# Performance work log

Measured on AMD Instinct MI355X. Metric: run time of the kernel, lower is better.

The kernel has to match this reference:

```python
import jax, jax.numpy as jnp
import numpy as np

INPUT_SIZE = 256
HIDDEN = 512

def setup_inputs() -> dict:
    key = jax.random.key(0)
    ks = jax.random.split(key, 12)
    B, T, I, H = 64, 1024, INPUT_SIZE, HIDDEN
    s = 1.0 / np.sqrt(I + H)
    x = jax.random.normal(ks[0], (B, T, I), dtype=jnp.float32)
    Wf = jax.random.uniform(ks[1], (I + H, H), jnp.float32, -s, s)
    bf = jax.random.uniform(ks[2], (H,), jnp.float32, -s, s)
    Wi = jax.random.uniform(ks[3], (I + H, H), jnp.float32, -s, s)
    bi = jax.random.uniform(ks[4], (H,), jnp.float32, -s, s)
    Wc = jax.random.uniform(ks[5], (I + H, H), jnp.float32, -s, s)
    bc = jax.random.uniform(ks[6], (H,), jnp.float32, -s, s)
    Wo = jax.random.uniform(ks[7], (I + H, H), jnp.float32, -s, s)
    bo = jax.random.uniform(ks[8], (H,), jnp.float32, -s, s)
    sf = 1.0 / np.sqrt(H)
    W_fc = jax.random.uniform(ks[9], (H, 1), jnp.float32, -sf, sf)
    b_fc = jax.random.uniform(ks[10], (1,), jnp.float32, -sf, sf)
    return {"x": x, "Wf": Wf, "bf": bf, "Wi": Wi, "bi": bi,
            "Wc": Wc, "bc": bc, "Wo": Wo, "bo": bo,
            "W_fc": W_fc, "b_fc": b_fc}

def reference(x, Wf, bf, Wi, bi, Wc, bc, Wo, bo, W_fc, b_fc):
    B, T, I = x.shape
    H = Wf.shape[1]
    # Fuse the 4 gate GEMMs into one [I+H, 4H] matmul (same math, one launch).
    W = jnp.concatenate([Wf, Wi, Wc, Wo], axis=1)   # [I+H, 4H]
    b = jnp.concatenate([bf, bi, bc, bo], axis=0)   # [4H]
    h0 = jnp.zeros((B, H), x.dtype)
    c0 = jnp.zeros((B, H), x.dtype)

    def step(carry, xt):
        h, c = carry
        combined = jnp.concatenate([xt, h], axis=1)     # [B, I+H]
        gates = combined @ W + b                        # [B, 4H]
        f, i, c_tilde, o = jnp.split(gates, 4, axis=1)
        f = jax.nn.sigmoid(f)
        i = jax.nn.sigmoid(i)
        c_tilde = jnp.tanh(c_tilde)
        o = jax.nn.sigmoid(o)
        c = f * c + i * c_tilde
        h = o * jnp.tanh(c)
        return (h, c), None

    (h, c), _ = jax.lax.scan(step, (h0, c0), jnp.swapaxes(x, 0, 1))
    return h @ W_fc + b_fc  # [B, 1]
```

## Files before the change

kernel.cpp:

```cpp
#include <hip/hip_runtime.h>
#include <hip/hip_fp16.h>


#define T_STEPS 1024
#define BATCH   64
#define ISZ     256
#define HSZ     512
#define NWG     128
#define NTHR    256
#define HB4     ((BATCH * HSZ) / 4)

typedef _Float16 half8  __attribute__((ext_vector_type(8)));
typedef _Float16 half4  __attribute__((ext_vector_type(4)));
typedef float    floatx4 __attribute__((ext_vector_type(4)));
typedef unsigned long long u64;

#define LD_AGENT(p)     __hip_atomic_load((p), __ATOMIC_RELAXED, __HIP_MEMORY_SCOPE_AGENT)
#define ST_AGENT(p, v)  __hip_atomic_store((p), (v), __ATOMIC_RELAXED, __HIP_MEMORY_SCOPE_AGENT)

__device__ __forceinline__ float fast_sigmoid(float x) {
    return 1.0f / (1.0f + __expf(-x));
}
__device__ __forceinline__ float fast_tanh(float x) {
    return 1.0f - 2.0f / (__expf(2.0f * x) + 1.0f);
}

__global__ __launch_bounds__(NTHR, 1) void lstm_persist(
    const float* __restrict__ x,
    const float* __restrict__ Wf, const float* __restrict__ bfv,
    const float* __restrict__ Wi, const float* __restrict__ biv,
    const float* __restrict__ Wc, const float* __restrict__ bcv,
    const float* __restrict__ Wo, const float* __restrict__ bov,
    u64* __restrict__ hbuf4, unsigned* __restrict__ flags)
{
    const int g    = blockIdx.x;
    const int tid  = threadIdx.x;
    const int w    = tid >> 6;
    const int l    = tid & 63;
    const int lj   = l & 15;
    const int lk   = l >> 4;
    const int gate = lj >> 2;
    const int jc   = lj & 3;
    const int hc   = (g << 2) + jc;
    const int row0 = w << 4;
    const int arow = row0 + lj;

    const float* Wg = (gate == 0) ? Wf : (gate == 1) ? Wi : (gate == 2) ? Wc : Wo;
    const float* bg = (gate == 0) ? bfv : (gate == 1) ? biv : (gate == 2) ? bcv : bov;

    half8 Bfrag[24];
    #pragma unroll
    for (int kf = 0; kf < 24; ++kf) {
        half8 v;
        #pragma unroll
        for (int e = 0; e < 8; ++e) {
            int k = (kf << 5) + (lk << 3) + e;
            v[e] = (_Float16)Wg[(size_t)k * HSZ + hc];
        }
        Bfrag[kf] = v;
    }
    const float bias = bg[hc];
    float cst[4] = {0.f, 0.f, 0.f, 0.f};

    const u64* fl = (const u64*)flags;

    floatx4 accx = {0.f, 0.f, 0.f, 0.f};
    {
        const float* xr = x + (size_t)arow * T_STEPS * ISZ + (lk << 3);
        #pragma unroll
        for (int kf = 0; kf < 8; ++kf) {
            floatx4 x0 = *(const floatx4*)(xr + (kf << 5));
            floatx4 x1 = *(const floatx4*)(xr + (kf << 5) + 4);
            half8 a;
            a[0] = (_Float16)x0[0]; a[1] = (_Float16)x0[1];
            a[2] = (_Float16)x0[2]; a[3] = (_Float16)x0[3];
            a[4] = (_Float16)x1[0]; a[5] = (_Float16)x1[1];
            a[6] = (_Float16)x1[2]; a[7] = (_Float16)x1[3];
            accx = __builtin_amdgcn_mfma_f32_16x16x32_f16(a, Bfrag[kf], accx, 0, 0, 0);
        }
    }

    for (int t = 0; t < T_STEPS; ++t) {
        floatx4 acc0, acc1;
        #pragma unroll
        for (int e = 0; e < 4; ++e) { acc0[e] = accx[e] + bias; acc1[e] = 0.f; }

        if (t > 0) {
            if (w == 0) {
                const unsigned tgt = (unsigned)t;
                while (true) {
                    u64 v = LD_AGENT(fl + l);
                    if (__all(((unsigned)v >= tgt) && ((unsigned)(v >> 32) >= tgt))) break;
                    __builtin_amdgcn_s_sleep(1);
                }
            }
            __syncthreads();

            const u64* hr = hbuf4 + (size_t)(t & 1) * HB4 + arow;
            u64 hl[32];
            #pragma unroll
            for (int kf = 0; kf < 16; ++kf) {
                const int c0 = kf * 8 + lk * 2;
                hl[2 * kf]     = LD_AGENT(hr + (size_t)c0 * BATCH);
                hl[2 * kf + 1] = LD_AGENT(hr + (size_t)(c0 + 1) * BATCH);
            }
            #pragma unroll
            for (int kf = 0; kf < 16; kf += 2) {
                union { u64 u[2]; half8 h; } a0, a1;
                a0.u[0] = hl[2 * kf];     a0.u[1] = hl[2 * kf + 1];
                a1.u[0] = hl[2 * kf + 2]; a1.u[1] = hl[2 * kf + 3];
                acc0 = __builtin_amdgcn_mfma_f32_16x16x32_f16(a0.h, Bfrag[8 + kf], acc0, 0, 0, 0);
                acc1 = __builtin_amdgcn_mfma_f32_16x16x32_f16(a1.h, Bfrag[9 + kf], acc1, 0, 0, 0);
            }
        }

        floatx4 act;
        if (gate == 2) {
            #pragma unroll
            for (int e = 0; e < 4; ++e) act[e] = fast_tanh(acc0[e] + acc1[e]);
        } else {
            #pragma unroll
            for (int e = 0; e < 4; ++e) act[e] = fast_sigmoid(acc0[e] + acc1[e]);
        }

        const int base = l & ~12;
        float hv[4];
        #pragma unroll
        for (int e = 0; e < 4; ++e) {
            float vf = __shfl(act[e], base);
            float vi = __shfl(act[e], base + 4);
            float vc = __shfl(act[e], base + 8);
            float vo = __shfl(act[e], base + 12);
            float c  = vf * cst[e] + vi * vc;
            cst[e] = c;
            hv[e] = vo * fast_tanh(c);
        }

        half4 outv;
        #pragma unroll
        for (int col = 0; col < 4; ++col) {
            const int src = ((l & 15) >> 2) * 16 + col;
            float sel = 0.f;
            #pragma unroll
            for (int e = 0; e < 4; ++e) {
                float tmp = __shfl(hv[e], src);
                if ((l & 3) == e) sel = tmp;
            }
            outv[col] = (_Float16)sel;
        }
        u64* hw = hbuf4 + (size_t)((t + 1) & 1) * HB4 + (size_t)g * BATCH + row0;
        if (l < 16) {
            union { half4 h; u64 u; } pk; pk.h = outv;
            ST_AGENT(hw + l, pk.u);
        }
        asm volatile("s_waitcnt vmcnt(0)" ::: "memory");
        __syncthreads();
        if (tid == 0) ST_AGENT(&flags[g], (unsigned)(t + 1));

        if (t + 1 < T_STEPS) {
            floatx4 az = {0.f, 0.f, 0.f, 0.f};
            const float* xr = x + ((size_t)arow * T_STEPS + (t + 1)) * ISZ + (lk << 3);
            #pragma unroll
            for (int kf = 0; kf < 8; ++kf) {
                floatx4 x0 = *(const floatx4*)(xr + (kf << 5));
                floatx4 x1 = *(const floatx4*)(xr + (kf << 5) + 4);
                half8 a;
                a[0] = (_Float16)x0[0]; a[1] = (_Float16)x0[1];
                a[2] = (_Float16)x0[2]; a[3] = (_Float16)x0[3];
                a[4] = (_Float16)x1[0]; a[5] = (_Float16)x1[1];
                a[6] = (_Float16)x1[2]; a[7] = (_Float16)x1[3];
                az = __builtin_amdgcn_mfma_f32_16x16x32_f16(a, Bfrag[kf], az, 0, 0, 0);
            }
            accx = az;
        }
    }
}

__global__ void out_proj(const u64* __restrict__ hb4, const float* __restrict__ Wfc,
                         const float* __restrict__ bfc, float* __restrict__ out)
{
    const int b = blockIdx.x;
    const int l = threadIdx.x;
    float s = 0.f;
    #pragma unroll
    for (int j = 0; j < 2; ++j) {
        const int c4 = l + (j << 6);
        union { u64 u; half4 h; } v;
        v.u = hb4[(size_t)c4 * BATCH + b];
        #pragma unroll
        for (int q = 0; q < 4; ++q)
            s += (float)v.h[q] * Wfc[c4 * 4 + q];
    }
    #pragma unroll
    for (int off = 32; off; off >>= 1) s += __shfl_down(s, off);
    if (l == 0) out[b] = s + bfc[0];
}

extern "C" void kernel_launch(void* const* d_in, const int* in_sizes, int n_in,
                              void* d_out, int out_size, void* d_ws, size_t ws_size,
                              hipStream_t stream)
{
    const float* x   = (const float*)d_in[0];
    const float* Wf  = (const float*)d_in[1];
    const float* bf  = (const float*)d_in[2];
    const float* Wi  = (const float*)d_in[3];
    const float* bi  = (const float*)d_in[4];
    const float* Wc  = (const float*)d_in[5];
    const float* bc  = (const float*)d_in[6];
    const float* Wo  = (const float*)d_in[7];
    const float* bo  = (const float*)d_in[8];
    const float* Wfc = (const float*)d_in[9];
    const float* bfc = (const float*)d_in[10];

    u64* hbuf4 = (u64*)d_ws;
    unsigned* flags = (unsigned*)((char*)d_ws + 2 * HB4 * sizeof(u64));

    hipMemsetAsync(flags, 0, NWG * sizeof(unsigned), stream);

    void* args[] = { (void*)&x, (void*)&Wf, (void*)&bf, (void*)&Wi, (void*)&bi,
                     (void*)&Wc, (void*)&bc, (void*)&Wo, (void*)&bo,
                     (void*)&hbuf4, (void*)&flags };
    hipLaunchCooperativeKernel((void*)lstm_persist, dim3(NWG), dim3(NTHR),
                               args, 0, stream);

    out_proj<<<dim3(BATCH), dim3(64), 0, stream>>>(hbuf4, Wfc, bfc, (float*)d_out);
}
```

Before: 4.749 ms.

## Replace per-step flag barrier with tagged h-data polling and triple buffering

Removes the per-step flag write, vmcnt wait and __syncthreads handoff. Each wave now polls the hidden-state buffer directly until every fp16 element carries the expected step tag, which is stored in its two low mantissa bits. A three-deep buffer plus per-wave progress counters stop a writer from overwriting a slot that slower consumers still need. The cooperative launch becomes a normal launch. This shortens the critical-path latency of each recurrent step, at the cost of two mantissa bits of h precision and more polling traffic.

```diff
diff --git a/kernel.cpp b/kernel.cpp
--- a/kernel.cpp
+++ b/kernel.cpp
@@ -9,6 +9,8 @@
 #define NWG     128
 #define NTHR    256
 #define HB4     ((BATCH * HSZ) / 4)
+#define NBUF    3
+#define TAGMASK 0x0003000300030003ULL
 
 typedef _Float16 half8  __attribute__((ext_vector_type(8)));
 typedef _Float16 half4  __attribute__((ext_vector_type(4)));
@@ -23,6 +25,10 @@
 }
 __device__ __forceinline__ float fast_tanh(float x) {
     return 1.0f - 2.0f / (__expf(2.0f * x) + 1.0f);
+}
+__device__ __forceinline__ u64 tagbits(int v) {
+    u64 d = (u64)(v & 3) | ((u64)((v >> 2) & 3) << 16);
+    return d | (d << 32);
 }
 
 __global__ __launch_bounds__(NTHR, 1) void lstm_persist(
@@ -31,7 +37,7 @@
     const float* __restrict__ Wi, const float* __restrict__ biv,
     const float* __restrict__ Wc, const float* __restrict__ bcv,
     const float* __restrict__ Wo, const float* __restrict__ bov,
-    u64* __restrict__ hbuf4, unsigned* __restrict__ flags)
+    u64* __restrict__ hbuf4, unsigned* __restrict__ pflags)
 {
     const int g    = blockIdx.x;
     const int tid  = threadIdx.x;
@@ -44,6 +50,7 @@
     const int hc   = (g << 2) + jc;
     const int row0 = w << 4;
     const int arow = row0 + lj;
+    const int pidx = (g << 2) + w;
 
     const float* Wg = (gate == 0) ? Wf : (gate == 1) ? Wi : (gate == 2) ? Wc : Wo;
     const float* bg = (gate == 0) ? bfv : (gate == 1) ? biv : (gate == 2) ? bcv : bov;
@@ -62,7 +69,7 @@
     const float bias = bg[hc];
     float cst[4] = {0.f, 0.f, 0.f, 0.f};
 
-    const u64* fl = (const u64*)flags;
+    const u64* pfl = (const u64*)pflags;
 
     floatx4 accx = {0.f, 0.f, 0.f, 0.f};
     {
@@ -80,30 +87,41 @@
         }
     }
 
+    unsigned minP_seen = 0;
+
     for (int t = 0; t < T_STEPS; ++t) {
+        u64 hl[32];
+        u64 pv[4] = {0, 0, 0, 0};
+        const bool need_guard = (t >= 3) && (minP_seen < (unsigned)(t - 2));
+
+        if (t > 0) {
+            const u64 expp = tagbits(((t - 1) % 15) + 1);
+            const u64* hr = hbuf4 + (size_t)(t % NBUF) * HB4 + arow;
+            for (;;) {
+                #pragma unroll
+                for (int kf = 0; kf < 16; ++kf) {
+                    const int c0 = kf * 8 + lk * 2;
+                    hl[2 * kf]     = LD_AGENT(hr + (size_t)c0 * BATCH);
+                    hl[2 * kf + 1] = LD_AGENT(hr + (size_t)(c0 + 1) * BATCH);
+                }
+                bool ok = true;
+                #pragma unroll
+                for (int i = 0; i < 32; ++i) ok &= ((hl[i] & TAGMASK) == expp);
+                if (__all(ok)) break;
+                __builtin_amdgcn_s_sleep(1);
+            }
+            if (l == 0) ST_AGENT(&pflags[pidx], (unsigned)t);
+            if (need_guard) {
+                #pragma unroll
+                for (int j = 0; j < 4; ++j) pv[j] = LD_AGENT(pfl + l + (j << 6));
+            }
+        }
+
         floatx4 acc0, acc1;
         #pragma unroll
         for (int e = 0; e < 4; ++e) { acc0[e] = accx[e] + bias; acc1[e] = 0.f; }
 
         if (t > 0) {
-            if (w == 0) {
-                const unsigned tgt = (unsigned)t;
-                while (true) {
-                    u64 v = LD_AGENT(fl + l);
-                    if (__all(((unsigned)v >= tgt) && ((unsigned)(v >> 32) >= tgt))) break;
-                    __builtin_amdgcn_s_sleep(1);
-                }
-            }
-            __syncthreads();
-
-            const u64* hr = hbuf4 + (size_t)(t & 1) * HB4 + arow;
-            u64 hl[32];
-            #pragma unroll
-            for (int kf = 0; kf < 16; ++kf) {
-                const int c0 = kf * 8 + lk * 2;
-                hl[2 * kf]     = LD_AGENT(hr + (size_t)c0 * BATCH);
-                hl[2 * kf + 1] = LD_AGENT(hr + (size_t)(c0 + 1) * BATCH);
-            }
             #pragma unroll
             for (int kf = 0; kf < 16; kf += 2) {
                 union { u64 u[2]; half8 h; } a0, a1;
@@ -148,14 +166,31 @@
             }
             outv[col] = (_Float16)sel;
         }
-        u64* hw = hbuf4 + (size_t)((t + 1) & 1) * HB4 + (size_t)g * BATCH + row0;
+
+        if (need_guard) {
+            const unsigned need = (unsigned)(t - 2);
+            for (;;) {
+                unsigned m = 0xffffffffu;
+                #pragma unroll
+                for (int j = 0; j < 4; ++j) {
+                    unsigned lo = (unsigned)pv[j], hi = (unsigned)(pv[j] >> 32);
+                    m = m < lo ? m : lo;
+                    m = m < hi ? m : hi;
+                }
+                if (__all(m >= need + 2)) { minP_seen = need + 2; break; }
+                if (__all(m >= need)) break;
+                __builtin_amdgcn_s_sleep(1);
+                #pragma unroll
+                for (int j = 0; j < 4; ++j) pv[j] = LD_AGENT(pfl + l + (j << 6));
+            }
+        }
+
+        u64* hw = hbuf4 + (size_t)((t + 1) % NBUF) * HB4 + (size_t)g * BATCH + row0;
         if (l < 16) {
             union { half4 h; u64 u; } pk; pk.h = outv;
+            pk.u = (pk.u & ~TAGMASK) | tagbits((t % 15) + 1);
             ST_AGENT(hw + l, pk.u);
         }
-        asm volatile("s_waitcnt vmcnt(0)" ::: "memory");
-        __syncthreads();
-        if (tid == 0) ST_AGENT(&flags[g], (unsigned)(t + 1));
 
         if (t + 1 < T_STEPS) {
             floatx4 az = {0.f, 0.f, 0.f, 0.f};
@@ -213,15 +248,15 @@
     const float* bfc = (const float*)d_in[10];
 
     u64* hbuf4 = (u64*)d_ws;
-    unsigned* flags = (unsigned*)((char*)d_ws + 2 * HB4 * sizeof(u64));
-
-    hipMemsetAsync(flags, 0, NWG * sizeof(unsigned), stream);
-
-    void* args[] = { (void*)&x, (void*)&Wf, (void*)&bf, (void*)&Wi, (void*)&bi,
-                     (void*)&Wc, (void*)&bc, (void*)&Wo, (void*)&bo,
-                     (void*)&hbuf4, (void*)&flags };
-    hipLaunchCooperativeKernel((void*)lstm_persist, dim3(NWG), dim3(NTHR),
-                               args, 0, stream);
-
-    out_proj<<<dim3(BATCH), dim3(64), 0, stream>>>(hbuf4, Wfc, bfc, (float*)d_out);
-}
+    unsigned* pflags = (unsigned*)((char*)d_ws + (size_t)NBUF * HB4 * sizeof(u64));
+
+    (void)hipMemsetAsync(hbuf4, 0,
+                         (size_t)NBUF * HB4 * sizeof(u64) + 512 * sizeof(unsigned),
+                         stream);
+
+    lstm_persist<<<dim3(NWG), dim3(NTHR), 0, stream>>>(
+        x, Wf, bf, Wi, bi, Wc, bc, Wo, bo, hbuf4, pflags);
+
+    const u64* hfinal = hbuf4 + (size_t)(T_STEPS % NBUF) * HB4;
+    out_proj<<<dim3(BATCH), dim3(64), 0, stream>>>(hfinal, Wfc, bfc, (float*)d_out);
+}
```

Result: slower. 7.454 ms (+57.0%).
